# Kernel tuning notes

Measured on AMD Instinct MI355X. Metric: run time of the kernel, lower is better.

The kernel has to match this reference:

```python
import jax, jax.numpy as jnp
import numpy as np

NUM_HEADS = 8

B, N, M = 2, 10000, 320000
QD = KD = HD = 256


def setup_inputs() -> dict:
    key = jax.random.key(0)
    k1, k2, k3, k4, k5 = jax.random.split(key, 5)
    x_q = jax.random.normal(k1, (B, N, QD), dtype=jnp.float32)
    x_k = jax.random.normal(k2, (B, N, KD), dtype=jnp.float32)
    mask = jax.random.randint(k3, (2, M), 0, N, dtype=jnp.int64)
    # xavier_uniform: limit = sqrt(6/(fan_in+fan_out))
    lim_q = float(np.sqrt(6.0 / (QD + HD)))
    lim_k = float(np.sqrt(6.0 / (KD + HD)))
    w_q = jax.random.uniform(k4, (QD, HD), minval=-lim_q, maxval=lim_q, dtype=jnp.float32)
    w_k = jax.random.uniform(k5, (KD, HD), minval=-lim_k, maxval=lim_k, dtype=jnp.float32)
    return {"x_q": x_q, "x_k": x_k, "mask": mask, "w_q": w_q, "w_k": w_k}


def reference(x_q, x_k, mask, w_q, w_k):
    b, n, _ = x_q.shape
    m = mask.shape[1]
    d = w_q.shape[1]          # hidden_dim
    h = NUM_HEADS
    dh = d // h
    q = x_q @ w_q             # (b, n, d)
    k = x_k @ w_k             # (b, n, d)
    # edge gather + elementwise multiply
    prod = q[:, mask[0], :] * k[:, mask[1], :]            # (b, m, d)
    # head buffer is i // (d/h): contiguous blocks -> reshape-sum
    a = prod.reshape(b, m, h, dh).sum(axis=-1)            # (b, m, h)
    a = a / jnp.sqrt(jnp.float32(w_k.shape[0]))           # / sqrt(key_dim)
    # segment softmax over destination index = mask[1 - reduce_dim], reduce_dim=1 -> mask[0]
    idx = mask[0]
    a = a - a.max()                                       # global max, as in source
    e = jnp.exp(a)                                        # (b, m, h)
    seg = jnp.zeros((b, n, h), e.dtype).at[:, idx, :].add(e)
    return e / (seg[:, idx, :] + 1e-16)
```

## Files before the change

### kernel.cpp

```cpp
#include <hip/hip_runtime.h>
#include <hip/hip_bf16.h>
#include <hip/hip_fp16.h>

#define DHID 256
#define NHEAD 8
#define BATCH 2

typedef _Float16 h8 __attribute__((ext_vector_type(8)));
typedef float f4 __attribute__((ext_vector_type(4)));

__global__ __launch_bounds__(256) void prep_kernel(
    const float* __restrict__ Wq, const float* __restrict__ Wk,
    _Float16* __restrict__ Wtq, _Float16* __restrict__ Wtk)
{
    const float* W = blockIdx.z ? Wk : Wq;
    _Float16* Wt   = blockIdx.z ? Wtk : Wtq;
    __shared__ float tile[32][33];
    const int tx = threadIdx.x;
    const int ty = threadIdx.y;
    const int n0 = blockIdx.x * 32;
    const int k0 = blockIdx.y * 32;
#pragma unroll
    for (int j = 0; j < 32; j += 8)
        tile[ty + j][tx] = W[(size_t)(k0 + ty + j) * DHID + n0 + tx];
    __syncthreads();
#pragma unroll
    for (int j = 0; j < 32; j += 8)
        Wt[(size_t)(n0 + ty + j) * DHID + k0 + tx] = (_Float16)tile[tx][ty + j];
}

__global__ __launch_bounds__(256, 2) void gemm_mfma(
    const float* __restrict__ Xq, const float* __restrict__ Xk,
    const _Float16* __restrict__ Wtq, const _Float16* __restrict__ Wtk,
    _Float16* __restrict__ Qh, _Float16* __restrict__ Kh,
    float* __restrict__ seg, int segN, int nx, int Mrows)
{
    const int t = threadIdx.x;
    if ((int)blockIdx.x >= nx) {
        if (blockIdx.z == 0) {
            int base = ((int)blockIdx.x - nx) * 256 + t;
            f4 z = {0.f, 0.f, 0.f, 0.f};
            for (int i = base; i < segN / 4; i += 8 * 256)
                ((f4*)seg)[i] = z;
        }
        return;
    }

    const float* X       = blockIdx.z ? Xk : Xq;
    const _Float16* Wt   = blockIdx.z ? Wtk : Wtq;
    _Float16* C          = blockIdx.z ? Kh : Qh;

    __shared__ _Float16 As[64 * 256];
    __shared__ _Float16 Bs[64 * 256];

    const int lane = t & 63;
    const int wave = t >> 6;
    const int rowBase = blockIdx.x * 64;

#pragma unroll
    for (int i = 0; i < 8; ++i) {
        int idx = t + i * 256;
        int row = idx >> 5;
        int c   = idx & 31;
        int grow = rowBase + row;
        f4 v0 = {0,0,0,0}, v1 = {0,0,0,0};
        if (grow < Mrows) {
            const float* p = X + (size_t)grow * DHID + c * 8;
            v0 = *(const f4*)p;
            v1 = *(const f4*)(p + 4);
        }
        h8 hv;
        hv[0]=(_Float16)v0[0]; hv[1]=(_Float16)v0[1]; hv[2]=(_Float16)v0[2]; hv[3]=(_Float16)v0[3];
        hv[4]=(_Float16)v1[0]; hv[5]=(_Float16)v1[1]; hv[6]=(_Float16)v1[2]; hv[7]=(_Float16)v1[3];
        int sc = c ^ (row & 7);
        *(h8*)&As[row * 256 + sc * 8] = hv;
    }

    const int ar   = wave * 16 + (lane & 15);
    const int quad = lane >> 4;

    for (int ct64 = 0; ct64 < 4; ++ct64) {
#pragma unroll
        for (int i = 0; i < 8; ++i) {
            int idx = t + i * 256;
            int n = idx >> 5;
            int c = idx & 31;
            h8 hv = *(const h8*)(Wt + (size_t)(ct64 * 64 + n) * DHID + c * 8);
            int sc = c ^ (n & 7);
            *(h8*)&Bs[n * 256 + sc * 8] = hv;
        }
        __syncthreads();

        f4 acc[4] = {{0,0,0,0},{0,0,0,0},{0,0,0,0},{0,0,0,0}};
#pragma unroll
        for (int kc = 0; kc < 8; ++kc) {
            int ac = (kc * 4 + quad) ^ (ar & 7);
            h8 afrag = *(const h8*)&As[ar * 256 + ac * 8];
#pragma unroll
            for (int ct = 0; ct < 4; ++ct) {
                int bn = ct * 16 + (lane & 15);
                int bc = (kc * 4 + quad) ^ (bn & 7);
                h8 bfrag = *(const h8*)&Bs[bn * 256 + bc * 8];
                acc[ct] = __builtin_amdgcn_mfma_f32_16x16x32_f16(afrag, bfrag, acc[ct], 0, 0, 0);
            }
        }

#pragma unroll
        for (int ct = 0; ct < 4; ++ct) {
#pragma unroll
            for (int r = 0; r < 4; ++r) {
                int grow = rowBase + wave * 16 + quad * 4 + r;
                if (grow < Mrows)
                    C[(size_t)grow * DHID + ct64 * 64 + ct * 16 + (lane & 15)] = (_Float16)acc[ct][r];
            }
        }
        __syncthreads();
    }
}

__global__ __launch_bounds__(256, 6) void edge_kernel(
    const _Float16* __restrict__ Qh, const _Float16* __restrict__ Kh,
    const int* __restrict__ mask, _Float16* __restrict__ eh,
    float* __restrict__ seg, int M, int N)
{
    const int lane = threadIdx.x & 63;
    const int wave = threadIdx.x >> 6;
    const int c    = lane & 31;
    const int half = lane >> 5;
    const int h    = c >> 2;
    const long e0 = ((long)blockIdx.x * 4 + wave) * 8;
    const int b = blockIdx.y;
    if (e0 >= M) return;

    int idxv = 0;
    {
        long le = e0 + (lane & 7);
        if (le >= M) le = M - 1;
        if (lane < 8)       idxv = mask[le];
        else if (lane < 16) idxv = mask[M + le];
    }

    const _Float16* Qb = Qh + (size_t)b * N * DHID;
    const _Float16* Kb = Kh + (size_t)b * N * DHID;

    int sidx[4], didx[4];
#pragma unroll
    for (int p = 0; p < 4; ++p) {
        sidx[p] = __shfl(idxv, p * 2 + half);
        didx[p] = __shfl(idxv, 8 + p * 2 + half);
    }

    h8 qv[4], kv[4];
#pragma unroll
    for (int p = 0; p < 4; ++p) {
        qv[p] = *(const h8*)(Qb + (size_t)sidx[p] * DHID + c * 8);
        kv[p] = *(const h8*)(Kb + (size_t)didx[p] * DHID + c * 8);
    }

#pragma unroll
    for (int p = 0; p < 4; ++p) {
        float s = 0.f;
#pragma unroll
        for (int u = 0; u < 8; ++u)
            s += (float)qv[p][u] * (float)kv[p][u];
        s += __shfl_xor(s, 1);
        s += __shfl_xor(s, 2);
        const long e = e0 + p * 2 + half;
        if ((c & 3) == 0 && e < M) {
            _Float16 evh = (_Float16)expf(s * 0.0625f);
            __builtin_nontemporal_store(evh, &eh[((size_t)b * M + e) * NHEAD + h]);
            atomicAdd(seg + ((size_t)b * N + sidx[p]) * NHEAD + h, (float)evh);
        }
    }
}

__global__ __launch_bounds__(256) void norm_kernel(
    const int* __restrict__ mask, const float* __restrict__ seg,
    const _Float16* __restrict__ eh, float* __restrict__ out,
    int M, int N, int BM)
{
    int idx = blockIdx.x * 256 + threadIdx.x;
    if (idx >= BM) return;
    int b = idx / M;
    int e = idx - b * M;
    int src = mask[e];
    const f4* s4 = (const f4*)(seg + ((size_t)b * N + src) * NHEAD);
    f4 s0 = s4[0], s1 = s4[1];
    h8 ev = *(const h8*)(eh + (size_t)idx * NHEAD);
    f4 o0, o1;
    o0[0] = (float)ev[0] * __builtin_amdgcn_rcpf(s0[0] + 1e-16f);
    o0[1] = (float)ev[1] * __builtin_amdgcn_rcpf(s0[1] + 1e-16f);
    o0[2] = (float)ev[2] * __builtin_amdgcn_rcpf(s0[2] + 1e-16f);
    o0[3] = (float)ev[3] * __builtin_amdgcn_rcpf(s0[3] + 1e-16f);
    o1[0] = (float)ev[4] * __builtin_amdgcn_rcpf(s1[0] + 1e-16f);
    o1[1] = (float)ev[5] * __builtin_amdgcn_rcpf(s1[1] + 1e-16f);
    o1[2] = (float)ev[6] * __builtin_amdgcn_rcpf(s1[2] + 1e-16f);
    o1[3] = (float)ev[7] * __builtin_amdgcn_rcpf(s1[3] + 1e-16f);
    f4* o4 = (f4*)(out + (size_t)idx * NHEAD);
    __builtin_nontemporal_store(o0, &o4[0]);
    __builtin_nontemporal_store(o1, &o4[1]);
}

extern "C" void kernel_launch(void* const* d_in, const int* in_sizes, int n_in,
                              void* d_out, int out_size, void* d_ws, size_t ws_size,
                              hipStream_t stream) {
    const float* x_q  = (const float*)d_in[0];
    const float* x_k  = (const float*)d_in[1];
    const int*   mask = (const int*)d_in[2];
    const float* w_q  = (const float*)d_in[3];
    const float* w_k  = (const float*)d_in[4];
    float* out = (float*)d_out;

    const int M = in_sizes[2] / 2;
    const int N = in_sizes[0] / (BATCH * DHID);
    const int Mrows = BATCH * N;
    const int segN  = BATCH * N * NHEAD;

    _Float16* Qh  = (_Float16*)d_ws;
    _Float16* Kh  = Qh  + (size_t)Mrows * DHID;
    _Float16* Wtq = Kh  + (size_t)Mrows * DHID;
    _Float16* Wtk = Wtq + (size_t)DHID * DHID;
    float*    seg = (float*)(Wtk + (size_t)DHID * DHID);
    _Float16* eh  = (_Float16*)(seg + (size_t)segN);

    prep_kernel<<<dim3(DHID / 32, DHID / 32, 2), dim3(32, 8), 0, stream>>>(
        w_q, w_k, Wtq, Wtk);

    const int nx = (Mrows + 63) / 64;
    gemm_mfma<<<dim3(nx + 8, 1, 2), 256, 0, stream>>>(
        x_q, x_k, Wtq, Wtk, Qh, Kh, seg, segN, nx, Mrows);

    long waves = (M + 7) / 8;
    dim3 egrid((unsigned)((waves + 3) / 4), BATCH);
    edge_kernel<<<egrid, 256, 0, stream>>>(Qh, Kh, mask, eh, seg, M, N);

    const int BM = BATCH * M;
    norm_kernel<<<(BM + 255) / 256, 256, 0, stream>>>(mask, seg, eh, out, M, N, BM);
}
```

Measured before the change: 182.0 us.

## Sort edges by source via counting sort to localize Q gathers and atomics

Adds a counting sort of the edges by source node: the prep kernel histograms the sources, a single-block scan builds offsets, and the spare gemm blocks scatter the edges into sorted src/dst/id arrays. The edge kernel then walks edges in source order, so Q reads and segment atomics for the same node sit close together and should hit cache more often, and it writes e values back at their original edge ids. It also switches the dot product to fdot2 and raises the occupancy hint. The cost is extra work: a memset, a serial one-block scan, atomic-based scattering and scattered eh writes.

```diff
diff --git a/kernel.cpp b/kernel.cpp
--- a/kernel.cpp
+++ b/kernel.cpp
@@ -7,12 +7,21 @@
 #define BATCH 2
 
 typedef _Float16 h8 __attribute__((ext_vector_type(8)));
+typedef _Float16 h2 __attribute__((ext_vector_type(2)));
 typedef float f4 __attribute__((ext_vector_type(4)));
 
 __global__ __launch_bounds__(256) void prep_kernel(
     const float* __restrict__ Wq, const float* __restrict__ Wk,
-    _Float16* __restrict__ Wtq, _Float16* __restrict__ Wtk)
-{
+    _Float16* __restrict__ Wtq, _Float16* __restrict__ Wtk,
+    const int* __restrict__ mask, int* __restrict__ cnt, int M)
+{
+    if (blockIdx.z == 2) {
+        const int tid = threadIdx.y * 32 + threadIdx.x;
+        const int bid = blockIdx.y * 8 + blockIdx.x;
+        for (int e = bid * 256 + tid; e < M; e += 64 * 256)
+            atomicAdd(&cnt[mask[e]], 1);
+        return;
+    }
     const float* W = blockIdx.z ? Wk : Wq;
     _Float16* Wt   = blockIdx.z ? Wtk : Wtq;
     __shared__ float tile[32][33];
@@ -29,19 +38,56 @@
         Wt[(size_t)(n0 + ty + j) * DHID + k0 + tx] = (_Float16)tile[tx][ty + j];
 }
 
+__global__ __launch_bounds__(1024) void scan_kernel(
+    const int* __restrict__ cnt, int* __restrict__ cur, int N)
+{
+    __shared__ int sums[1024];
+    const int t = threadIdx.x;
+    const int per = (N + 1023) >> 10;
+    const int base = t * per;
+    int s = 0;
+    for (int i = 0; i < per; ++i) {
+        int j = base + i;
+        if (j < N) s += cnt[j];
+    }
+    sums[t] = s;
+    __syncthreads();
+    for (int off = 1; off < 1024; off <<= 1) {
+        int v = (t >= off) ? sums[t - off] : 0;
+        __syncthreads();
+        sums[t] += v;
+        __syncthreads();
+    }
+    int run = (t == 0) ? 0 : sums[t - 1];
+    for (int i = 0; i < per; ++i) {
+        int j = base + i;
+        if (j < N) { cur[j] = run; run += cnt[j]; }
+    }
+}
+
 __global__ __launch_bounds__(256, 2) void gemm_mfma(
     const float* __restrict__ Xq, const float* __restrict__ Xk,
     const _Float16* __restrict__ Wtq, const _Float16* __restrict__ Wtk,
     _Float16* __restrict__ Qh, _Float16* __restrict__ Kh,
-    float* __restrict__ seg, int segN, int nx, int Mrows)
+    float* __restrict__ seg, int segN, int nx, int Mrows,
+    const int* __restrict__ mask, int* __restrict__ cur,
+    int* __restrict__ ssrc, int* __restrict__ sdst, int* __restrict__ seid,
+    int M)
 {
     const int t = threadIdx.x;
     if ((int)blockIdx.x >= nx) {
+        const int sb = (int)blockIdx.x - nx;
         if (blockIdx.z == 0) {
-            int base = ((int)blockIdx.x - nx) * 256 + t;
             f4 z = {0.f, 0.f, 0.f, 0.f};
-            for (int i = base; i < segN / 4; i += 8 * 256)
+            for (int i = sb * 256 + t; i < segN / 4; i += 64 * 256)
                 ((f4*)seg)[i] = z;
+        } else {
+            for (int e = sb * 256 + t; e < M; e += 64 * 256) {
+                int s = mask[e];
+                int d = mask[M + e];
+                int pos = atomicAdd(&cur[s], 1);
+                ssrc[pos] = s; sdst[pos] = d; seid[pos] = e;
+            }
         }
         return;
     }
@@ -118,9 +164,10 @@
     }
 }
 
-__global__ __launch_bounds__(256, 6) void edge_kernel(
+__global__ __launch_bounds__(256, 8) void edge_kernel(
     const _Float16* __restrict__ Qh, const _Float16* __restrict__ Kh,
-    const int* __restrict__ mask, _Float16* __restrict__ eh,
+    const int* __restrict__ ssrc, const int* __restrict__ sdst,
+    const int* __restrict__ seid, _Float16* __restrict__ eh,
     float* __restrict__ seg, int M, int N)
 {
     const int lane = threadIdx.x & 63;
@@ -136,39 +183,52 @@
     {
         long le = e0 + (lane & 7);
         if (le >= M) le = M - 1;
-        if (lane < 8)       idxv = mask[le];
-        else if (lane < 16) idxv = mask[M + le];
+        if (lane < 8)       idxv = ssrc[le];
+        else if (lane < 16) idxv = sdst[le];
+        else if (lane < 24) idxv = seid[le];
     }
 
     const _Float16* Qb = Qh + (size_t)b * N * DHID;
     const _Float16* Kb = Kh + (size_t)b * N * DHID;
 
-    int sidx[4], didx[4];
+    int sidx[4], didx[4], eidx[4];
 #pragma unroll
     for (int p = 0; p < 4; ++p) {
         sidx[p] = __shfl(idxv, p * 2 + half);
         didx[p] = __shfl(idxv, 8 + p * 2 + half);
+        eidx[p] = __shfl(idxv, 16 + p * 2 + half);
     }
 
     h8 qv[4], kv[4];
 #pragma unroll
-    for (int p = 0; p < 4; ++p) {
+    for (int p = 0; p < 4; ++p)
+        kv[p] = *(const h8*)(Kb + (size_t)didx[p] * DHID + c * 8);
+#pragma unroll
+    for (int p = 0; p < 4; ++p)
         qv[p] = *(const h8*)(Qb + (size_t)sidx[p] * DHID + c * 8);
-        kv[p] = *(const h8*)(Kb + (size_t)didx[p] * DHID + c * 8);
-    }
 
 #pragma unroll
     for (int p = 0; p < 4; ++p) {
         float s = 0.f;
+#if __has_builtin(__builtin_amdgcn_fdot2)
+#pragma unroll
+        for (int u = 0; u < 4; ++u) {
+            h2 a, bb;
+            a[0]  = qv[p][2 * u]; a[1]  = qv[p][2 * u + 1];
+            bb[0] = kv[p][2 * u]; bb[1] = kv[p][2 * u + 1];
+            s = __builtin_amdgcn_fdot2(a, bb, s, false);
+        }
+#else
 #pragma unroll
         for (int u = 0; u < 8; ++u)
             s += (float)qv[p][u] * (float)kv[p][u];
+#endif
         s += __shfl_xor(s, 1);
         s += __shfl_xor(s, 2);
         const long e = e0 + p * 2 + half;
         if ((c & 3) == 0 && e < M) {
             _Float16 evh = (_Float16)expf(s * 0.0625f);
-            __builtin_nontemporal_store(evh, &eh[((size_t)b * M + e) * NHEAD + h]);
+            eh[((size_t)b * M + eidx[p]) * NHEAD + h] = evh;
             atomicAdd(seg + ((size_t)b * N + sidx[p]) * NHEAD + h, (float)evh);
         }
     }
@@ -222,17 +282,27 @@
     _Float16* Wtk = Wtq + (size_t)DHID * DHID;
     float*    seg = (float*)(Wtk + (size_t)DHID * DHID);
     _Float16* eh  = (_Float16*)(seg + (size_t)segN);
-
-    prep_kernel<<<dim3(DHID / 32, DHID / 32, 2), dim3(32, 8), 0, stream>>>(
-        w_q, w_k, Wtq, Wtk);
+    int*      cnt = (int*)(eh + (size_t)BATCH * M * NHEAD);
+    int*      cur = cnt + N;
+    int*      ssrc = cur + N;
+    int*      sdst = ssrc + M;
+    int*      seid = sdst + M;
+
+    hipMemsetAsync(cnt, 0, (size_t)N * sizeof(int), stream);
+
+    prep_kernel<<<dim3(DHID / 32, DHID / 32, 3), dim3(32, 8), 0, stream>>>(
+        w_q, w_k, Wtq, Wtk, mask, cnt, M);
+
+    scan_kernel<<<1, 1024, 0, stream>>>(cnt, cur, N);
 
     const int nx = (Mrows + 63) / 64;
-    gemm_mfma<<<dim3(nx + 8, 1, 2), 256, 0, stream>>>(
-        x_q, x_k, Wtq, Wtk, Qh, Kh, seg, segN, nx, Mrows);
+    gemm_mfma<<<dim3(nx + 64, 1, 2), 256, 0, stream>>>(
+        x_q, x_k, Wtq, Wtk, Qh, Kh, seg, segN, nx, Mrows,
+        mask, cur, ssrc, sdst, seid, M);
 
     long waves = (M + 7) / 8;
     dim3 egrid((unsigned)((waves + 3) / 4), BATCH);
-    edge_kernel<<<egrid, 256, 0, stream>>>(Qh, Kh, mask, eh, seg, M, N);
+    edge_kernel<<<egrid, 256, 0, stream>>>(Qh, Kh, ssrc, sdst, seid, eh, seg, M, N);
 
     const int BM = BATCH * M;
     norm_kernel<<<(BM + 255) / 256, 256, 0, stream>>>(mask, seg, eh, out, M, N, BM);
```

Result: slower. 274.3 us (+50.7%).
